# Kernel tuning notes

Hardware: AMD Instinct MI355X
Metric: run time of the kernel (lower is better)

## Reference

```python
import jax, jax.numpy as jnp
import numpy as np

FEAT_DIM = 2048
NUM_CLASSES = 30000
BATCH = 1024
CLAMP_MIN = 1e-12
CLAMP_MAX = 1.0e12


def setup_inputs() -> dict:
    key = jax.random.key(0)
    k1, k2, k3 = jax.random.split(key, 3)
    x = jax.random.normal(k1, (BATCH, FEAT_DIM), dtype=jnp.float32)
    labels = jax.random.randint(k2, (BATCH,), 0, NUM_CLASSES, dtype=jnp.int64)
    centers = jax.random.normal(k3, (NUM_CLASSES, FEAT_DIM), dtype=jnp.float32)
    return {"x": x, "labels": labels, "centers": centers}


def reference(x, labels, centers):
    # Original builds distmat[b, c] = (||x_b||^2 + ||c_c||^2 - 2 x_b . c_c) / feat_dim
    # and then gathers only the true-class column per row. We gather the needed
    # centers first (same math, avoids materializing the [B, C] distmat).
    feat_dim = x.shape[1]
    cy = centers[labels]                                  # [B, D]
    dist = (jnp.sum(x * x, axis=1)
            + jnp.sum(cy * cy, axis=1)
            - 2.0 * jnp.sum(x * cy, axis=1)) / feat_dim    # [B]
    dist = jnp.clip(dist, CLAMP_MIN, CLAMP_MAX)
    return jnp.mean(dist)
```

## Files before the change

### kernel.cpp

```cpp
#include <hip/hip_runtime.h>

#define FEAT_DIM 2048
#define BATCH 1024
#define CLAMP_MIN 1e-12f
#define CLAMP_MAX 1e12f

__global__ void __launch_bounds__(256) center_dist_kernel(
    const float* __restrict__ x,
    const int* __restrict__ labels,
    const float* __restrict__ centers,
    float* __restrict__ row_dist) {
    const int b = blockIdx.x;
    const int t = threadIdx.x;

    const float4* xr = reinterpret_cast<const float4*>(x + (size_t)b * FEAT_DIM);
    const int lab = labels[b];
    const float4* cr = reinterpret_cast<const float4*>(centers + (size_t)lab * FEAT_DIM);

    float acc = 0.0f;
#pragma unroll
    for (int i = 0; i < FEAT_DIM / 4 / 256; ++i) {
        const int idx = t + i * 256;
        const float4 xv = xr[idx];
        const float4 cv = cr[idx];
        const float dx = xv.x - cv.x;
        const float dy = xv.y - cv.y;
        const float dz = xv.z - cv.z;
        const float dw = xv.w - cv.w;
        acc += dx * dx + dy * dy + dz * dz + dw * dw;
    }

#pragma unroll
    for (int off = 32; off > 0; off >>= 1)
        acc += __shfl_down(acc, off, 64);

    __shared__ float wave_sums[4];
    const int wid = t >> 6;
    const int lane = t & 63;
    if (lane == 0) wave_sums[wid] = acc;
    __syncthreads();
    if (t == 0) {
        const float s = wave_sums[0] + wave_sums[1] + wave_sums[2] + wave_sums[3];
        row_dist[b] = s * (1.0f / (float)FEAT_DIM);
    }
}

__global__ void __launch_bounds__(256) center_reduce_kernel(
    const float* __restrict__ row_dist,
    float* __restrict__ out) {
    const int t = threadIdx.x;
    float acc = 0.0f;
#pragma unroll
    for (int i = 0; i < BATCH / 256; ++i) {
        float d = row_dist[t + i * 256];
        d = fminf(fmaxf(d, CLAMP_MIN), CLAMP_MAX);
        acc += d;
    }
#pragma unroll
    for (int off = 32; off > 0; off >>= 1)
        acc += __shfl_down(acc, off, 64);

    __shared__ float wave_sums[4];
    const int wid = t >> 6;
    const int lane = t & 63;
    if (lane == 0) wave_sums[wid] = acc;
    __syncthreads();
    if (t == 0) {
        out[0] = (wave_sums[0] + wave_sums[1] + wave_sums[2] + wave_sums[3]) *
                 (1.0f / (float)BATCH);
    }
}

extern "C" void kernel_launch(void* const* d_in, const int* in_sizes, int n_in,
                              void* d_out, int out_size, void* d_ws, size_t ws_size,
                              hipStream_t stream) {
    const float* x = (const float*)d_in[0];
    const int* labels = (const int*)d_in[1];
    const float* centers = (const float*)d_in[2];
    float* out = (float*)d_out;
    float* row_dist = (float*)d_ws;

    center_dist_kernel<<<BATCH, 256, 0, stream>>>(x, labels, centers, row_dist);
    center_reduce_kernel<<<1, 256, 0, stream>>>(row_dist, out);
}
```

Measured before the change: 11.28 us.

## Fuse row distance and mean reduction into one kernel with atomic accumulation

Merges the per-row distance kernel and the final reduction kernel into one launch. Each wavefront now handles one full row instead of four wavefronts sharing it, and each block clamps and sums its four rows before an atomicAdd into the output, which is zeroed first with a memset. The goal is to remove the second kernel launch and the workspace round trip. In exchange it adds a memset node, 256 atomics on a single address, and a float sum whose order is no longer deterministic.

```diff
diff --git a/kernel.cpp b/kernel.cpp
--- a/kernel.cpp
+++ b/kernel.cpp
@@ -5,69 +5,55 @@
 #define CLAMP_MIN 1e-12f
 #define CLAMP_MAX 1e12f
 
-__global__ void __launch_bounds__(256) center_dist_kernel(
+#define ROWS_PER_BLOCK 4
+#define NBLOCKS (BATCH / ROWS_PER_BLOCK)
+
+__global__ void __launch_bounds__(256) center_loss_fused_kernel(
     const float* __restrict__ x,
     const int* __restrict__ labels,
     const float* __restrict__ centers,
-    float* __restrict__ row_dist) {
-    const int b = blockIdx.x;
+    float* __restrict__ out) {
     const int t = threadIdx.x;
+    const int wid = t >> 6;
+    const int lane = t & 63;
+    const int row = blockIdx.x * ROWS_PER_BLOCK + wid;
 
-    const float4* xr = reinterpret_cast<const float4*>(x + (size_t)b * FEAT_DIM);
-    const int lab = labels[b];
+    const float4* xr = reinterpret_cast<const float4*>(x + (size_t)row * FEAT_DIM);
+    const int lab = labels[row];
     const float4* cr = reinterpret_cast<const float4*>(centers + (size_t)lab * FEAT_DIM);
 
-    float acc = 0.0f;
+    float a0 = 0.0f, a1 = 0.0f;
 #pragma unroll
-    for (int i = 0; i < FEAT_DIM / 4 / 256; ++i) {
-        const int idx = t + i * 256;
-        const float4 xv = xr[idx];
-        const float4 cv = cr[idx];
-        const float dx = xv.x - cv.x;
-        const float dy = xv.y - cv.y;
-        const float dz = xv.z - cv.z;
-        const float dw = xv.w - cv.w;
-        acc += dx * dx + dy * dy + dz * dz + dw * dw;
+    for (int i = 0; i < FEAT_DIM / 4 / 64; i += 2) {
+        const float4 xv0 = xr[lane + i * 64];
+        const float4 cv0 = cr[lane + i * 64];
+        const float4 xv1 = xr[lane + (i + 1) * 64];
+        const float4 cv1 = cr[lane + (i + 1) * 64];
+        const float d0x = xv0.x - cv0.x, d0y = xv0.y - cv0.y;
+        const float d0z = xv0.z - cv0.z, d0w = xv0.w - cv0.w;
+        const float d1x = xv1.x - cv1.x, d1y = xv1.y - cv1.y;
+        const float d1z = xv1.z - cv1.z, d1w = xv1.w - cv1.w;
+        a0 += d0x * d0x + d0y * d0y + d0z * d0z + d0w * d0w;
+        a1 += d1x * d1x + d1y * d1y + d1z * d1z + d1w * d1w;
     }
+    float acc = a0 + a1;
 
 #pragma unroll
     for (int off = 32; off > 0; off >>= 1)
         acc += __shfl_down(acc, off, 64);
 
-    __shared__ float wave_sums[4];
-    const int wid = t >> 6;
-    const int lane = t & 63;
+    __shared__ float wave_sums[ROWS_PER_BLOCK];
     if (lane == 0) wave_sums[wid] = acc;
     __syncthreads();
     if (t == 0) {
-        const float s = wave_sums[0] + wave_sums[1] + wave_sums[2] + wave_sums[3];
-        row_dist[b] = s * (1.0f / (float)FEAT_DIM);
-    }
-}
-
-__global__ void __launch_bounds__(256) center_reduce_kernel(
-    const float* __restrict__ row_dist,
-    float* __restrict__ out) {
-    const int t = threadIdx.x;
-    float acc = 0.0f;
+        float block_sum = 0.0f;
 #pragma unroll
-    for (int i = 0; i < BATCH / 256; ++i) {
-        float d = row_dist[t + i * 256];
-        d = fminf(fmaxf(d, CLAMP_MIN), CLAMP_MAX);
-        acc += d;
-    }
-#pragma unroll
-    for (int off = 32; off > 0; off >>= 1)
-        acc += __shfl_down(acc, off, 64);
-
-    __shared__ float wave_sums[4];
-    const int wid = t >> 6;
-    const int lane = t & 63;
-    if (lane == 0) wave_sums[wid] = acc;
-    __syncthreads();
-    if (t == 0) {
-        out[0] = (wave_sums[0] + wave_sums[1] + wave_sums[2] + wave_sums[3]) *
-                 (1.0f / (float)BATCH);
+        for (int w = 0; w < ROWS_PER_BLOCK; ++w) {
+            float d = wave_sums[w] * (1.0f / (float)FEAT_DIM);
+            d = fminf(fmaxf(d, CLAMP_MIN), CLAMP_MAX);
+            block_sum += d;
+        }
+        atomicAdd(out, block_sum * (1.0f / (float)BATCH));
     }
 }
 
@@ -78,8 +64,7 @@
     const int* labels = (const int*)d_in[1];
     const float* centers = (const float*)d_in[2];
     float* out = (float*)d_out;
-    float* row_dist = (float*)d_ws;
 
-    center_dist_kernel<<<BATCH, 256, 0, stream>>>(x, labels, centers, row_dist);
-    center_reduce_kernel<<<1, 256, 0, stream>>>(row_dist, out);
+    hipMemsetAsync(out, 0, sizeof(float), stream);
+    center_loss_fused_kernel<<<NBLOCKS, 256, 0, stream>>>(x, labels, centers, out);
 }
```

Result: slower. 14.64 us (+29.8%).
